# Optimization experiments

Hardware: AMD Instinct MI355X
Metric: run time of the kernel (lower is better)

The kernel has to match this reference:

```python
import math
import jax, jax.numpy as jnp
import numpy as np

ONE_SIDED_W = 256   # attention_window // 2
NUM_HEADS = 12


def _sliding_window_attention(q, k, v, w):
    """q,k,v: [B,H,S,D]; each query attends keys in [i-w, i+w]. q pre-scaled."""
    B, H, S, D = q.shape
    C = S // w  # number of query chunks of size w
    # pad keys/values by w on each side of the sequence dim
    kp = jnp.pad(k, ((0, 0), (0, 0), (w, w), (0, 0)))
    vp = jnp.pad(v, ((0, 0), (0, 0), (w, w), (0, 0)))
    # for query chunk c, key window covers padded positions [c*w, c*w+3w)
    idx3 = jnp.arange(C)[:, None] * w + jnp.arange(3 * w)[None, :]  # [C,3w]
    k3 = kp[:, :, idx3]  # [B,H,C,3w,D]
    v3 = vp[:, :, idx3]  # [B,H,C,3w,D]
    qc = q.reshape(B, H, C, w, D)
    scores3 = jnp.einsum('bhcxd,bhcyd->bhcxy', qc, k3)  # [B,H,C,w,3w]
    # extract the diagonal band: rel offset j in [0, 2w] maps to window col x+j
    xi = jnp.arange(w)[:, None]            # [w,1]
    ji = jnp.arange(2 * w + 1)[None, :]    # [1,2w+1]
    yi = xi + ji                           # [w,2w+1]
    band = scores3[:, :, :, xi, yi]        # [B,H,C,w,2w+1]
    # mask keys falling outside the real sequence (boundary -inf masking)
    kidx = (jnp.arange(C)[:, None, None] - 1) * w + yi[None]  # global key index
    valid = (kidx >= 0) & (kidx < S)       # [C,w,2w+1]
    band = jnp.where(valid[None, None], band, -jnp.inf)
    probs = jax.nn.softmax(band, axis=-1)  # every row has >= w+1 valid keys
    # scatter band probs back to [w,3w] per chunk, then banded matmul with v3
    full = jnp.zeros((B, H, C, w, 3 * w), q.dtype).at[:, :, :, xi, yi].set(probs)
    ctx = jnp.einsum('bhcxy,bhcyd->bhcxd', full, v3)  # [B,H,C,w,D]
    return ctx.reshape(B, H, S, D)


def setup_inputs() -> dict:
    key = jax.random.key(0)
    ks = jax.random.split(key, 7)
    B, S, E = 2, 4096, 768
    hs = jax.random.normal(ks[0], (B, S, E), dtype=jnp.float32)
    mk = lambda k: jax.random.normal(k, (E, E), dtype=jnp.float32) * 0.02
    return {
        'hidden_states': hs,
        'q_w': mk(ks[1]), 'q_b': jnp.zeros((E,), jnp.float32),
        'k_w': mk(ks[2]), 'k_b': jnp.zeros((E,), jnp.float32),
        'v_w': mk(ks[3]), 'v_b': jnp.zeros((E,), jnp.float32),
    }


def reference(hidden_states, q_w, q_b, k_w, k_b, v_w, v_b):
    B, S, E = hidden_states.shape
    H = NUM_HEADS
    D = E // H
    w = ONE_SIDED_W
    q = (hidden_states @ q_w.T + q_b) / math.sqrt(D)
    k = hidden_states @ k_w.T + k_b
    v = hidden_states @ v_w.T + v_b
    # [B,S,E] -> [B,H,S,D]
    q = q.reshape(B, S, H, D).transpose(0, 2, 1, 3)
    k = k.reshape(B, S, H, D).transpose(0, 2, 1, 3)
    v = v.reshape(B, S, H, D).transpose(0, 2, 1, 3)
    ctx = _sliding_window_attention(q, k, v, w)  # [B,H,S,D]
    return ctx.transpose(0, 2, 1, 3).reshape(B, S, E)
```

## Files before the change

kernel.cpp:

```cpp
#include <hip/hip_runtime.h>
#include <math.h>

#define NB 2
#define NS 4096
#define NE 768
#define NH 12
#define ND 64
#define NW 256
#define GK NE

typedef __attribute__((ext_vector_type(8))) short short8v;
typedef __attribute__((ext_vector_type(4))) float f32x4;

__device__ __forceinline__ unsigned short f2bf(float f) {
    unsigned u = __float_as_uint(f);
    u += 0x7FFFu + ((u >> 16) & 1u);
    return (unsigned short)(u >> 16);
}

#if __has_builtin(__builtin_amdgcn_global_load_lds)
#define HAVE_GLL 1
#else
#define HAVE_GLL 0
#endif

__global__ __launch_bounds__(256)
void convert_bf16(const float* __restrict__ hs, const float* __restrict__ qw,
                  const float* __restrict__ kw, const float* __restrict__ vw,
                  unsigned short* __restrict__ hsb, unsigned short* __restrict__ Wb)
{
    const int NU_HS = (NB * NS * NE) / 4;
    const int NU_W  = (NE * NE) / 4;
    const int total = NU_HS + 3 * NU_W;
    for (int u = blockIdx.x * 256 + threadIdx.x; u < total; u += gridDim.x * 256) {
        const float4* src;
        unsigned short* dst;
        if (u < NU_HS) {
            src = (const float4*)hs + u;
            dst = hsb + (size_t)u * 4;
        } else {
            int v = u - NU_HS;
            int m = v / NU_W;
            int r = v - m * NU_W;
            const float* wp = (m == 0) ? qw : (m == 1) ? kw : vw;
            src = (const float4*)wp + r;
            dst = Wb + (size_t)m * (NE * NE) + (size_t)r * 4;
        }
        float4 f = *src;
        ushort4 o;
        o.x = f2bf(f.x); o.y = f2bf(f.y); o.z = f2bf(f.z); o.w = f2bf(f.w);
        *(ushort4*)dst = o;
    }
}

__global__ __launch_bounds__(256, 3)
void qkv_mfma(const unsigned short* __restrict__ hsb, const unsigned short* __restrict__ Wb,
              const float* __restrict__ qb, const float* __restrict__ kb,
              const float* __restrict__ vb,
              unsigned short* __restrict__ Qg, unsigned short* __restrict__ Kg,
              unsigned short* __restrict__ Vt)
{
    __shared__ unsigned short lA[128 * 64];
    __shared__ unsigned short lB[128 * 64];

    const int t  = threadIdx.x;
    const int w  = t >> 6;
    const int l  = t & 63;

    const int lin = blockIdx.x + (blockIdx.y << 6);
    const int nl  = (lin & 7) * 144 + (lin >> 3);
    const int bm  = nl & 63;
    const int bn  = nl >> 6;

    const int mat = bn / 6;
    const int n0  = (bn % 6) * 128;
    const int m0  = bm * 128;

    const unsigned short* Wm = Wb + (size_t)mat * (NE * NE);

    const int srow = l >> 3;
    const int scol = (((l & 7) ^ srow) << 3);

    const int lw   = l & 15;
    const int lk16 = (l >> 4) << 4;
    const int swz  = (l & 7) << 4;
    const int r0   = (w >> 1) * 64;
    const int c0   = (w & 1) * 64;

    f32x4 acc[4][4] = {};

    for (int kt = 0; kt < GK / 64; ++kt) {
        const int k0 = kt * 64;
        __syncthreads();
#pragma unroll
        for (int i = 0; i < 4; ++i) {
            const int rowA = m0 + 32 * w + 8 * i + srow;
            const int rowB = n0 + 32 * w + 8 * i + srow;
            const unsigned short* ga = hsb + (size_t)rowA * GK + k0 + scol;
            const unsigned short* gb = Wm  + (size_t)rowB * GK + k0 + scol;
#if HAVE_GLL
            __builtin_amdgcn_global_load_lds(
                (const __attribute__((address_space(1))) void*)ga,
                (__attribute__((address_space(3))) void*)&lA[(32 * w + 8 * i) * 64], 16, 0, 0);
            __builtin_amdgcn_global_load_lds(
                (const __attribute__((address_space(1))) void*)gb,
                (__attribute__((address_space(3))) void*)&lB[(32 * w + 8 * i) * 64], 16, 0, 0);
#else
            *(short8v*)&lA[(32 * w + 8 * i) * 64 + l * 8] = *(const short8v*)ga;
            *(short8v*)&lB[(32 * w + 8 * i) * 64 + l * 8] = *(const short8v*)gb;
#endif
        }
        __syncthreads();

        const unsigned short* rT = (mat < 2) ? lB : lA;
        const unsigned short* cT = (mat < 2) ? lA : lB;

#pragma unroll
        for (int kk = 0; kk < 2; ++kk) {
            const int pb = (((kk * 64) + lk16) ^ swz) >> 1;
            short8v a[4], b[4];
#pragma unroll
            for (int r = 0; r < 4; ++r)
                a[r] = *(const short8v*)&rT[(r0 + r * 16 + lw) * 64 + pb];
#pragma unroll
            for (int c = 0; c < 4; ++c)
                b[c] = *(const short8v*)&cT[(c0 + c * 16 + lw) * 64 + pb];
#pragma unroll
            for (int r = 0; r < 4; ++r)
#pragma unroll
                for (int c = 0; c < 4; ++c)
                    acc[r][c] = __builtin_amdgcn_mfma_f32_16x16x32_bf16(a[r], b[c], acc[r][c], 0, 0, 0);
        }
    }

    const float* bias = (mat == 0) ? qb : (mat == 1) ? kb : vb;
    const float scale = (mat == 0) ? 0.125f : 1.0f;

    if (mat < 2) {
        unsigned short* Out = (mat == 0) ? Qg : Kg;
#pragma unroll
        for (int r = 0; r < 4; ++r) {
            const int nf0 = n0 + r0 + r * 16 + ((l >> 4) << 2);
            const float4 b4 = *(const float4*)&bias[nf0];
            const int h  = nf0 >> 6;
            const int d0 = nf0 & 63;
#pragma unroll
            for (int c = 0; c < 4; ++c) {
                const int m  = m0 + c0 + c * 16 + lw;
                const int bb = m >> 12;
                const int s  = m & (NS - 1);
                ushort4 o;
                o.x = f2bf((acc[r][c][0] + b4.x) * scale);
                o.y = f2bf((acc[r][c][1] + b4.y) * scale);
                o.z = f2bf((acc[r][c][2] + b4.z) * scale);
                o.w = f2bf((acc[r][c][3] + b4.w) * scale);
                *(ushort4*)&Out[((size_t)(bb * NH + h) * NS + s) * ND + d0] = o;
            }
        }
    } else {
#pragma unroll
        for (int c = 0; c < 4; ++c) {
            const int nf = n0 + c0 + c * 16 + lw;
            const float bs = bias[nf];
            const int h = nf >> 6;
            const int d = nf & 63;
#pragma unroll
            for (int r = 0; r < 4; ++r) {
                const int m  = m0 + r0 + r * 16 + ((l >> 4) << 2);
                const int bb = m >> 12;
                const int s0 = m & (NS - 1);
                ushort4 o;
                o.x = f2bf(acc[r][c][0] + bs);
                o.y = f2bf(acc[r][c][1] + bs);
                o.z = f2bf(acc[r][c][2] + bs);
                o.w = f2bf(acc[r][c][3] + bs);
                *(ushort4*)&Vt[((size_t)(bb * NH + h) * ND + d) * NS + s0] = o;
            }
        }
    }
}

__global__ __launch_bounds__(256, 3)
void swattn_mfma(const unsigned short* __restrict__ Qg, const unsigned short* __restrict__ Kg,
                 const unsigned short* __restrict__ Vt, float* __restrict__ out)
{
    __shared__ unsigned short Ks[64 * 72];
    __shared__ unsigned short Vs[64 * 72];
    __shared__ unsigned short Ps[4][16 * 72];

    const int t  = threadIdx.x;
    const int w  = t >> 6;
    const int l  = t & 63;

    const int blk0 = blockIdx.x;
    const int blk  = (blk0 & 7) * 192 + (blk0 >> 3);
    const int qt   = blk & 63;
    const int bh   = blk >> 6;
    const int i0   = qt * 64;

    const unsigned short* Qp = Qg + (size_t)bh * NS * ND;
    const unsigned short* Kp = Kg + (size_t)bh * NS * ND;
    const unsigned short* Vp = Vt + (size_t)bh * ND * NS;

    const int lw = l & 15;
    const int g4 = l >> 4;

    short8v aq[2];
#pragma unroll
    for (int kk = 0; kk < 2; ++kk)
        aq[kk] = *(const short8v*)&Qp[(size_t)(i0 + w * 16 + lw) * ND + kk * 32 + g4 * 8];

    f32x4 cacc[4] = {};
    float l_part[4] = {0.f, 0.f, 0.f, 0.f};

    for (int kt = 0; kt < 9; ++kt) {
        const int kj0 = i0 - NW + kt * 64;
        if (kj0 < 0 || kj0 >= NS) continue;

        __syncthreads();
#pragma unroll
        for (int r = 0; r < 2; ++r) {
            const int u   = t + 256 * r;
            const int row = u >> 3;
            const int c8  = (u & 7) * 8;
            *(short8v*)&Ks[row * 72 + c8] = *(const short8v*)&Kp[(size_t)(kj0 + row) * ND + c8];
            *(short8v*)&Vs[row * 72 + c8] = *(const short8v*)&Vp[(size_t)row * NS + kj0 + c8];
        }
        __syncthreads();

        f32x4 sc[4];
#pragma unroll
        for (int cf = 0; cf < 4; ++cf) {
            f32x4 z = {0.f, 0.f, 0.f, 0.f};
#pragma unroll
            for (int kk = 0; kk < 2; ++kk) {
                short8v b = *(const short8v*)&Ks[(cf * 16 + lw) * 72 + kk * 32 + g4 * 8];
                z = __builtin_amdgcn_mfma_f32_16x16x32_bf16(aq[kk], b, z, 0, 0, 0);
            }
            sc[cf] = z;
        }

        if (kt == 0) {
#pragma unroll
            for (int cf = 0; cf < 4; ++cf) {
                const int lk = cf * 16 + lw;
#pragma unroll
                for (int j = 0; j < 4; ++j)
                    if (lk < w * 16 + g4 * 4 + j) sc[cf][j] = -1e30f;
            }
        } else if (kt == 8) {
#pragma unroll
            for (int cf = 0; cf < 4; ++cf) {
                const int lk = cf * 16 + lw;
#pragma unroll
                for (int j = 0; j < 4; ++j)
                    if (lk > w * 16 + g4 * 4 + j) sc[cf][j] = -1e30f;
            }
        }

        float p[4][4];
#pragma unroll
        for (int cf = 0; cf < 4; ++cf)
#pragma unroll
            for (int j = 0; j < 4; ++j)
                p[cf][j] = __expf(sc[cf][j]);
#pragma unroll
        for (int j = 0; j < 4; ++j)
            l_part[j] += (p[0][j] + p[1][j]) + (p[2][j] + p[3][j]);

        unsigned short* Pw = Ps[w];
#pragma unroll
        for (int cf = 0; cf < 4; ++cf)
#pragma unroll
            for (int j = 0; j < 4; ++j)
                Pw[(g4 * 4 + j) * 72 + cf * 16 + lw] = f2bf(p[cf][j]);

#pragma unroll
        for (int kk = 0; kk < 2; ++kk) {
            short8v pa = *(const short8v*)&Pw[lw * 72 + kk * 32 + g4 * 8];
#pragma unroll
            for (int df = 0; df < 4; ++df) {
                short8v bv = *(const short8v*)&Vs[(df * 16 + lw) * 72 + kk * 32 + g4 * 8];
                cacc[df] = __builtin_amdgcn_mfma_f32_16x16x32_bf16(pa, bv, cacc[df], 0, 0, 0);
            }
        }
    }

    float l_run[4];
#pragma unroll
    for (int j = 0; j < 4; ++j) {
        float sm = l_part[j];
        sm += __shfl_xor(sm, 1);
        sm += __shfl_xor(sm, 2);
        sm += __shfl_xor(sm, 4);
        sm += __shfl_xor(sm, 8);
        l_run[j] = sm;
    }

    const int bb = bh / NH;
    const int h  = bh - bb * NH;
#pragma unroll
    for (int j = 0; j < 4; ++j) {
        const float inv = 1.f / l_run[j];
        const int s = i0 + w * 16 + g4 * 4 + j;
        float* op = out + ((size_t)bb * NS + s) * NE + h * ND + lw;
#pragma unroll
        for (int df = 0; df < 4; ++df)
            op[df * 16] = cacc[df][j] * inv;
    }
}

extern "C" void kernel_launch(void* const* d_in, const int* in_sizes, int n_in,
                              void* d_out, int out_size, void* d_ws, size_t ws_size,
                              hipStream_t stream) {
    const float* hs = (const float*)d_in[0];
    const float* qw = (const float*)d_in[1];
    const float* qb = (const float*)d_in[2];
    const float* kw = (const float*)d_in[3];
    const float* kb = (const float*)d_in[4];
    const float* vw = (const float*)d_in[5];
    const float* vb = (const float*)d_in[6];
    float* out = (float*)d_out;

    unsigned short* hsb = (unsigned short*)d_ws;
    unsigned short* Wb  = hsb + (size_t)NB * NS * NE;
    unsigned short* Qg  = Wb + 3 * NE * NE;
    unsigned short* Kg  = Qg + (size_t)NB * NH * NS * ND;
    unsigned short* Vg  = Kg + (size_t)NB * NH * NS * ND;

    convert_bf16<<<1968, 256, 0, stream>>>(hs, qw, kw, vw, hsb, Wb);
    qkv_mfma<<<dim3(64, 18), 256, 0, stream>>>(hsb, Wb, qb, kb, vb, Qg, Kg, Vg);
    swattn_mfma<<<NB * NH * (NS / 64), 256, 0, stream>>>(Qg, Kg, Vg, out);
}
```

Baseline: 171.8 us.

## Load K/V fragments directly from global in attention; remap QKV GEMM block order

The attention kernel stops staging K and V tiles in LDS behind two barriers per key tile. Each wave now reads its MFMA operand fragments straight from global memory and relies on L2/L1 caching, because all four waves read the same tile. Separately, the QKV GEMM moves to a 1D grid with a new block-to-tile mapping that groups 8 M-tiles per XCD sharing each N-tile, aiming for better L2 reuse. The cost is four times more global or cache traffic for K/V, with possibly uncoalesced 16-byte reads, in exchange for no barriers and less LDS.

```diff
diff --git a/kernel.cpp b/kernel.cpp
--- a/kernel.cpp
+++ b/kernel.cpp
@@ -67,10 +67,11 @@
     const int w  = t >> 6;
     const int l  = t & 63;
 
-    const int lin = blockIdx.x + (blockIdx.y << 6);
-    const int nl  = (lin & 7) * 144 + (lin >> 3);
-    const int bm  = nl & 63;
-    const int bn  = nl >> 6;
+    const int lin = blockIdx.x;
+    const int xcd = lin & 7;
+    const int i   = lin >> 3;
+    const int bm  = xcd * 8 + (i & 7);
+    const int bn  = i >> 3;
 
     const int mat = bn / 6;
     const int n0  = (bn % 6) * 128;
@@ -93,21 +94,21 @@
         const int k0 = kt * 64;
         __syncthreads();
 #pragma unroll
-        for (int i = 0; i < 4; ++i) {
-            const int rowA = m0 + 32 * w + 8 * i + srow;
-            const int rowB = n0 + 32 * w + 8 * i + srow;
+        for (int ii = 0; ii < 4; ++ii) {
+            const int rowA = m0 + 32 * w + 8 * ii + srow;
+            const int rowB = n0 + 32 * w + 8 * ii + srow;
             const unsigned short* ga = hsb + (size_t)rowA * GK + k0 + scol;
             const unsigned short* gb = Wm  + (size_t)rowB * GK + k0 + scol;
 #if HAVE_GLL
             __builtin_amdgcn_global_load_lds(
                 (const __attribute__((address_space(1))) void*)ga,
-                (__attribute__((address_space(3))) void*)&lA[(32 * w + 8 * i) * 64], 16, 0, 0);
+                (__attribute__((address_space(3))) void*)&lA[(32 * w + 8 * ii) * 64], 16, 0, 0);
             __builtin_amdgcn_global_load_lds(
                 (const __attribute__((address_space(1))) void*)gb,
-                (__attribute__((address_space(3))) void*)&lB[(32 * w + 8 * i) * 64], 16, 0, 0);
+                (__attribute__((address_space(3))) void*)&lB[(32 * w + 8 * ii) * 64], 16, 0, 0);
 #else
-            *(short8v*)&lA[(32 * w + 8 * i) * 64 + l * 8] = *(const short8v*)ga;
-            *(short8v*)&lB[(32 * w + 8 * i) * 64 + l * 8] = *(const short8v*)gb;
+            *(short8v*)&lA[(32 * w + 8 * ii) * 64 + l * 8] = *(const short8v*)ga;
+            *(short8v*)&lB[(32 * w + 8 * ii) * 64 + l * 8] = *(const short8v*)gb;
 #endif
         }
         __syncthreads();
@@ -184,8 +185,6 @@
 void swattn_mfma(const unsigned short* __restrict__ Qg, const unsigned short* __restrict__ Kg,
                  const unsigned short* __restrict__ Vt, float* __restrict__ out)
 {
-    __shared__ unsigned short Ks[64 * 72];
-    __shared__ unsigned short Vs[64 * 72];
     __shared__ unsigned short Ps[4][16 * 72];
 
     const int t  = threadIdx.x;
@@ -217,24 +216,13 @@
         const int kj0 = i0 - NW + kt * 64;
         if (kj0 < 0 || kj0 >= NS) continue;
 
-        __syncthreads();
-#pragma unroll
-        for (int r = 0; r < 2; ++r) {
-            const int u   = t + 256 * r;
-            const int row = u >> 3;
-            const int c8  = (u & 7) * 8;
-            *(short8v*)&Ks[row * 72 + c8] = *(const short8v*)&Kp[(size_t)(kj0 + row) * ND + c8];
-            *(short8v*)&Vs[row * 72 + c8] = *(const short8v*)&Vp[(size_t)row * NS + kj0 + c8];
-        }
-        __syncthreads();
-
         f32x4 sc[4];
 #pragma unroll
         for (int cf = 0; cf < 4; ++cf) {
             f32x4 z = {0.f, 0.f, 0.f, 0.f};
 #pragma unroll
             for (int kk = 0; kk < 2; ++kk) {
-                short8v b = *(const short8v*)&Ks[(cf * 16 + lw) * 72 + kk * 32 + g4 * 8];
+                short8v b = *(const short8v*)&Kp[(size_t)(kj0 + cf * 16 + lw) * ND + kk * 32 + g4 * 8];
                 z = __builtin_amdgcn_mfma_f32_16x16x32_bf16(aq[kk], b, z, 0, 0, 0);
             }
             sc[cf] = z;
@@ -280,7 +268,7 @@
             short8v pa = *(const short8v*)&Pw[lw * 72 + kk * 32 + g4 * 8];
 #pragma unroll
             for (int df = 0; df < 4; ++df) {
-                short8v bv = *(const short8v*)&Vs[(df * 16 + lw) * 72 + kk * 32 + g4 * 8];
+                short8v bv = *(const short8v*)&Vp[(size_t)(df * 16 + lw) * NS + kj0 + kk * 32 + g4 * 8];
                 cacc[df] = __builtin_amdgcn_mfma_f32_16x16x32_bf16(pa, bv, cacc[df], 0, 0, 0);
             }
         }
@@ -329,6 +317,6 @@
     unsigned short* Vg  = Kg + (size_t)NB * NH * NS * ND;
 
     convert_bf16<<<1968, 256, 0, stream>>>(hs, qw, kw, vw, hsb, Wb);
-    qkv_mfma<<<dim3(64, 18), 256, 0, stream>>>(hsb, Wb, qb, kb, vb, Qg, Kg, Vg);
+    qkv_mfma<<<1152, 256, 0, stream>>>(hsb, Wb, qb, kb, vb, Qg, Kg, Vg);
     swattn_mfma<<<NB * NH * (NS / 64), 256, 0, stream>>>(Qg, Kg, Vg, out);
 }
```

Result: slower. 243.9 us (+42.0%).
